# Kernel optimization log

Hardware: AMD Instinct MI355X
Metric: run time of the kernel (lower is better)

## Reference

```python
import jax, jax.numpy as jnp
import numpy as np

N_NODES = 100000
N_EDGES = 1_600_000


def _glorot(key, shape):
    fan_in, fan_out = shape
    s = jnp.sqrt(6.0 / (fan_in + fan_out)).astype(jnp.float32)
    return jax.random.uniform(key, shape, jnp.float32, -1.0, 1.0) * s


def setup_inputs() -> dict:
    key = jax.random.key(0)
    ks = jax.random.split(key, 6)
    x = jax.random.normal(ks[0], (N_NODES, 88), jnp.float32)
    edge_index = jax.random.randint(ks[1], (2, N_EDGES), 0, N_NODES, dtype=jnp.int32)
    return {
        "x": x,
        "W1": _glorot(ks[2], (88, 65)), "b1": jnp.zeros((65,), jnp.float32),
        "W2": _glorot(ks[3], (65, 50)), "b2": jnp.zeros((50,), jnp.float32),
        "W3": _glorot(ks[4], (50, 65)), "b3": jnp.zeros((65,), jnp.float32),
        "W4": _glorot(ks[5], (65, 88)), "b4": jnp.zeros((88,), jnp.float32),
        "edge_index": edge_index,
    }


def _gcn_conv(h, W, b, src, dst, norm, n):
    # PyG GCNConv: transform, then normalized neighbor aggregation (self-loops
    # already folded into src/dst/norm).
    h = h @ W                                  # [N, out]
    msg = h[src] * norm[:, None]               # [E+N, out] gather
    return jax.ops.segment_sum(msg, dst, num_segments=n) + b  # scatter-add


def reference(x, W1, b1, W2, b2, W3, b3, W4, b4, edge_index):
    n = x.shape[0]
    loop = jnp.arange(n, dtype=edge_index.dtype)
    src = jnp.concatenate([edge_index[0], loop])   # add self-loops
    dst = jnp.concatenate([edge_index[1], loop])
    deg = jax.ops.segment_sum(jnp.ones_like(dst, dtype=x.dtype), dst, num_segments=n)
    dinv = jnp.where(deg > 0, jax.lax.rsqrt(deg), 0.0)
    norm = dinv[src] * dinv[dst]                   # D^-1/2 (A+I) D^-1/2 edge weights

    # encoder
    h = jax.nn.relu(_gcn_conv(x, W1, b1, src, dst, norm, n))
    h = _gcn_conv(h, W2, b2, src, dst, norm, n)
    # decoder
    h = jax.nn.relu(_gcn_conv(h, W3, b3, src, dst, norm, n))
    return _gcn_conv(h, W4, b4, src, dst, norm, n)
```

## Files before the change

### kernel.cpp

```cpp
#include <hip/hip_runtime.h>

#define BS 256
#define FB 1024
#define NB 256
#define CHUNK 4096
#define CAP 64
#define LCAP 8192

using half8 = __attribute__((ext_vector_type(8))) _Float16;

template<typename T>
__device__ __forceinline__ void load8f(const T* p, float (&d)[8]) {
    if constexpr (sizeof(T) == 4) {
        float4 a = *(const float4*)p;
        float4 b = *(const float4*)(p + 4);
        d[0] = a.x; d[1] = a.y; d[2] = a.z; d[3] = a.w;
        d[4] = b.x; d[5] = b.y; d[6] = b.z; d[7] = b.w;
    } else {
        half8 v = *(const half8*)p;
        #pragma unroll
        for (int j = 0; j < 8; ++j) d[j] = (float)v[j];
    }
}
template<typename T>
__device__ __forceinline__ void store8f(T* p, const float (&d)[8]) {
    if constexpr (sizeof(T) == 4) {
        *(float4*)p       = make_float4(d[0], d[1], d[2], d[3]);
        *(float4*)(p + 4) = make_float4(d[4], d[5], d[6], d[7]);
    } else {
        half8 h;
        #pragma unroll
        for (int j = 0; j < 8; ++j) h[j] = (_Float16)d[j];
        *(half8*)p = h;
    }
}


__global__ __launch_bounds__(BS) void k_bucket(const int* __restrict__ src, const int* __restrict__ dst,
                                               unsigned* __restrict__ bbuf, int* __restrict__ bcounts,
                                               int E, unsigned long long invB, int bsz) {
    __shared__ int lcnt[NB];
    for (int t = threadIdx.x; t < NB; t += BS) lcnt[t] = 0;
    __syncthreads();
    int base_e = blockIdx.x * CHUNK;
    unsigned* mybuf = bbuf + (size_t)blockIdx.x * NB * CAP;
    #pragma unroll
    for (int j = 0; j < CHUNK / BS; ++j) {
        int e = base_e + j * BS + threadIdx.x;
        if (e < E) {
            int d = dst[e];
            int s = src[e];
            int b = (int)(((unsigned long long)(unsigned)d * invB) >> 40);
            int doff = d - b * bsz;
            int pos = atomicAdd(&lcnt[b], 1);
            if (pos < CAP)
                mybuf[b * CAP + pos] = ((unsigned)doff << 17) | (unsigned)s;
        }
    }
    __syncthreads();
    for (int t = threadIdx.x; t < NB; t += BS)
        bcounts[blockIdx.x * NB + t] = min(lcnt[t], CAP);
}

__global__ __launch_bounds__(FB) void k_cnt(const unsigned* __restrict__ bbuf, const int* __restrict__ bcounts,
                                            int* __restrict__ cnt, int nch, int bsz, int N) {
    __shared__ int lhist[512];
    for (int t = threadIdx.x; t < 512; t += FB) lhist[t] = 0;
    __syncthreads();
    int b = blockIdx.x;
    int lo = b * bsz;
    int total = nch * CAP;
    for (int idx = threadIdx.x; idx < total; idx += FB) {
        int seg = idx >> 6, slot = idx & 63;
        int c = bcounts[seg * NB + b];
        if (slot < c)
            atomicAdd(&lhist[bbuf[((size_t)seg * NB + b) * CAP + slot] >> 17], 1);
    }
    __syncthreads();
    int hi = min(N, lo + bsz);
    for (int t = threadIdx.x; t < hi - lo; t += FB) cnt[lo + t] = lhist[t];
}

__global__ __launch_bounds__(BS) void k_scan1(const int* __restrict__ cnt, int* __restrict__ bsum,
                                              float* __restrict__ dinv, int N) {
    __shared__ int s[BS];
    int i = blockIdx.x * BS + threadIdx.x;
    int v = (i < N) ? cnt[i] : 0;
    if (i < N) dinv[i] = rsqrtf((float)(v + 1));
    s[threadIdx.x] = v;
    __syncthreads();
    for (int off = BS / 2; off > 0; off >>= 1) {
        if (threadIdx.x < off) s[threadIdx.x] += s[threadIdx.x + off];
        __syncthreads();
    }
    if (threadIdx.x == 0) bsum[blockIdx.x] = s[0];
}

__global__ __launch_bounds__(512) void k_scan2(int* bsum, int nb) {
    __shared__ int s[512];
    int t = threadIdx.x;
    int v = (t < nb) ? bsum[t] : 0;
    s[t] = v;
    __syncthreads();
    for (int off = 1; off < 512; off <<= 1) {
        int u = (t >= off) ? s[t - off] : 0;
        __syncthreads();
        s[t] += u;
        __syncthreads();
    }
    if (t < nb) bsum[t] = s[t] - v;
}

__global__ __launch_bounds__(BS) void k_scan3(const int* __restrict__ cnt, const int* __restrict__ boff,
                                              int* __restrict__ row_ptr, int N) {
    __shared__ int s[BS];
    int t = threadIdx.x;
    int i = blockIdx.x * BS + t;
    int v = (i < N) ? cnt[i] : 0;
    s[t] = v;
    __syncthreads();
    for (int off = 1; off < BS; off <<= 1) {
        int u = (t >= off) ? s[t - off] : 0;
        __syncthreads();
        s[t] += u;
        __syncthreads();
    }
    int base = boff[blockIdx.x];
    if (i < N) row_ptr[i] = base + s[t] - v;
    if (i == N - 1) row_ptr[N] = base + s[t];
}

__global__ __launch_bounds__(FB) void k_fill2(const unsigned* __restrict__ bbuf, const int* __restrict__ bcounts,
                                              const int* __restrict__ row_ptr, const float* __restrict__ dinv,
                                              uint2* __restrict__ entries,
                                              int nch, int bsz, int N) {
    __shared__ int cur[512];
    __shared__ float ldinv[512];
    __shared__ unsigned sorted[LCAP];

    int b = blockIdx.x;
    int lo = b * bsz;
    int hi = min(N, lo + bsz);
    int gbase = row_ptr[lo];
    int tot = row_ptr[hi] - gbase;
    for (int t = threadIdx.x; t < hi - lo; t += FB) {
        cur[t] = row_ptr[lo + t] - gbase;
        ldinv[t] = dinv[lo + t];
    }
    __syncthreads();

    int total = nch * CAP;
    for (int idx = threadIdx.x; idx < total; idx += FB) {
        int seg = idx >> 6, slot = idx & 63;
        int c = bcounts[seg * NB + b];
        if (slot < c) {
            unsigned u = bbuf[((size_t)seg * NB + b) * CAP + slot];
            int p = atomicAdd(&cur[u >> 17], 1);
            if (p < LCAP) sorted[p] = u;
        }
    }
    __syncthreads();

    for (int t = threadIdx.x; t < tot; t += FB) {
        unsigned u = sorted[t];
        int s = (int)(u & 0x1FFFFu);
        int doff = (int)(u >> 17);
        float w = dinv[s] * ldinv[doff];
        entries[gbase + t] = make_uint2((unsigned)s, __float_as_uint(w));
    }
}

template<typename TIN, int K, int M, int LDIN, int LDOUT, bool BIAS, bool RELU, typename TOUT>
__global__ __launch_bounds__(BS) void k_gemm(const TIN* __restrict__ H, const float* __restrict__ Wg,
                                             const float* __restrict__ bias, TOUT* __restrict__ out, int N) {
    constexpr int M8 = (M + 7) & ~7;
    constexpr int CG = M8 / 8;
    constexpr int WSTR = K * 8 + 4;
    __shared__ float Wl[CG * WSTR];
    for (int idx = threadIdx.x; idx < CG * WSTR; idx += BS) {
        int cg = idx / WSTR, rem = idx - cg * WSTR;
        int k = rem >> 3, j = rem & 7;
        int m = cg * 8 + j;
        Wl[idx] = (rem < K * 8 && m < M) ? Wg[(size_t)k * M + m] : 0.f;
    }
    __syncthreads();

    int nrq = (N + 3) >> 2;
    int idx = blockIdx.x * BS + threadIdx.x;
    if (idx >= nrq * CG) return;
    int rq = idx / CG;
    int cg = idx - rq * CG;
    int c0 = cg * 8;
    int r0 = rq * 4;
    const float* wb = &Wl[cg * WSTR];

    const TIN* h[4];
    #pragma unroll
    for (int r = 0; r < 4; ++r) {
        int rr = r0 + r; rr = (rr < N) ? rr : (N - 1);
        h[r] = H + (size_t)rr * LDIN;
    }

    float acc[4][8];
    #pragma unroll
    for (int r = 0; r < 4; ++r)
        #pragma unroll
        for (int m = 0; m < 8; ++m) acc[r][m] = 0.f;

    constexpr int K8 = K & ~7;
    #pragma unroll 1
    for (int k = 0; k < K8; k += 8) {
        float p[4][8];
        load8f(h[0] + k, p[0]);
        load8f(h[1] + k, p[1]);
        load8f(h[2] + k, p[2]);
        load8f(h[3] + k, p[3]);
        const float* wl = wb + k * 8;
        #pragma unroll
        for (int j = 0; j < 8; ++j) {
            float4 wa = *(const float4*)(wl + j * 8);
            float4 wc = *(const float4*)(wl + j * 8 + 4);
            const float wv[8] = {wa.x, wa.y, wa.z, wa.w, wc.x, wc.y, wc.z, wc.w};
            #pragma unroll
            for (int r = 0; r < 4; ++r)
                #pragma unroll
                for (int m = 0; m < 8; ++m)
                    acc[r][m] = fmaf(p[r][j], wv[m], acc[r][m]);
        }
    }
    #pragma unroll
    for (int k = K8; k < K; ++k) {
        const float* wl = wb + k * 8;
        float4 wa = *(const float4*)(wl);
        float4 wc = *(const float4*)(wl + 4);
        const float wv[8] = {wa.x, wa.y, wa.z, wa.w, wc.x, wc.y, wc.z, wc.w};
        #pragma unroll
        for (int r = 0; r < 4; ++r) {
            float pv = (float)h[r][k];
            #pragma unroll
            for (int m = 0; m < 8; ++m)
                acc[r][m] = fmaf(pv, wv[m], acc[r][m]);
        }
    }

    #pragma unroll
    for (int r = 0; r < 4; ++r) {
        int rr = r0 + r;
        if (rr >= N) break;
        float v[8];
        #pragma unroll
        for (int m = 0; m < 8; ++m) {
            int c = c0 + m;
            bool in = (c < M);
            float x = in ? acc[r][m] : 0.f;
            if (BIAS && in) x += bias[c];
            if (RELU) x = fmaxf(x, 0.f);
            v[m] = x;
        }
        store8f(out + (size_t)rr * LDOUT + c0, v);
    }
}

template<typename TIN, typename TOUT, int M, int M8, int LDI, int LDO, bool BIAS, bool RELU>
__global__ __launch_bounds__(BS) void k_agg(const TIN* __restrict__ T, TOUT* __restrict__ out,
                                            const int* __restrict__ row_ptr, const uint2* __restrict__ entries,
                                            const float* __restrict__ dinv, const float* __restrict__ bias,
                                            int N) {
    constexpr int CG = M8 / 8;
    int idx = blockIdx.x * BS + threadIdx.x;
    if (idx >= N * CG) return;
    int i  = idx / CG;
    int cg = idx - i * CG;
    int c0 = cg * 8;

    float di = dinv[i];
    float w0 = di * di;
    float t0[8];
    load8f(T + (size_t)i * LDI + c0, t0);
    float a0[8], a1[8];
    #pragma unroll
    for (int m = 0; m < 8; ++m) { a0[m] = w0 * t0[m]; a1[m] = 0.f; }

    int e0 = row_ptr[i], e1 = row_ptr[i + 1];
    for (int e = e0; e < e1; e += 8) {
        unsigned sidx[8];
        float w[8];
        #pragma unroll
        for (int j = 0; j < 8; ++j) {
            int ee = e + j;
            int ec = (ee < e1) ? ee : (e1 - 1);
            uint2 u = entries[ec];
            sidx[j] = u.x;
            w[j] = (ee < e1) ? __uint_as_float(u.y) : 0.f;
        }
        #pragma unroll
        for (int j = 0; j < 8; ++j) {
            float g[8];
            load8f(T + (size_t)sidx[j] * LDI + c0, g);
            if (j & 1) {
                #pragma unroll
                for (int m = 0; m < 8; ++m) a1[m] = fmaf(w[j], g[m], a1[m]);
            } else {
                #pragma unroll
                for (int m = 0; m < 8; ++m) a0[m] = fmaf(w[j], g[m], a0[m]);
            }
        }
    }

    #pragma unroll
    for (int m = 0; m < 8; ++m) {
        float v = a0[m] + a1[m];
        if (BIAS && (c0 + m) < M) v += bias[c0 + m];
        if (RELU) v = fmaxf(v, 0.f);
        a0[m] = v;
    }
    store8f(out + (size_t)i * LDO + c0, a0);
}


extern "C" void kernel_launch(void* const* d_in, const int* in_sizes, int n_in,
                              void* d_out, int out_size, void* d_ws, size_t ws_size,
                              hipStream_t stream) {
    const float* x  = (const float*)d_in[0];
    const float* W1 = (const float*)d_in[1];
    const float* b1 = (const float*)d_in[2];
    const float* W2 = (const float*)d_in[3];
    const float* b2 = (const float*)d_in[4];
    const float* W3 = (const float*)d_in[5];
    const float* b3 = (const float*)d_in[6];
    const float* W4 = (const float*)d_in[7];
    const float* b4 = (const float*)d_in[8];
    const int* edge_index = (const int*)d_in[9];

    const int N = in_sizes[0] / 88;
    const int E = in_sizes[9] / 2;
    const int* src = edge_index;
    const int* dst = edge_index + E;

    const int nch = (E + CHUNK - 1) / CHUNK;
    const int bsz = (N + NB - 1) / NB;
    const unsigned long long invB = ((1ull << 40) + bsz - 1) / bsz;

    auto al = [](size_t b) { return (b + 255) & ~(size_t)255; };
    char* p = (char*)d_ws;
    auto carve = [&](size_t bytes) { void* r = p; p += (bytes + 255) & ~(size_t)255; return r; };
    int*   cnt     = (int*)  carve((size_t)N * 4);
    float* dinv    = (float*)carve((size_t)N * 4);
    int*   row_ptr = (int*)  carve((size_t)(N + 1) * 4);
    int*   bsum    = (int*)  carve(4096);
    uint2* entries = (uint2*)carve((size_t)E * 8);

    char* ub = p;
    int*      bcounts = (int*)ub;
    unsigned* bbuf    = (unsigned*)(ub + al((size_t)nch * NB * 4));
    size_t csr_bytes  = al((size_t)nch * NB * 4) + al((size_t)nch * NB * CAP * 4);

    size_t hbytes = al((size_t)N * 72 * 2);
    _Float16* hA = (_Float16*)ub;
    _Float16* hB = (_Float16*)(ub + hbytes);
    _Float16* hC = (_Float16*)(ub + 2 * hbytes);
    size_t h_bytes_tot = 3 * hbytes;

    p = ub + (csr_bytes > h_bytes_tot ? csr_bytes : h_bytes_tot);
    (void)p; (void)ws_size;

    int gN = (N + BS - 1) / BS;

    k_bucket<<<nch, BS, 0, stream>>>(src, dst, bbuf, bcounts, E, invB, bsz);
    k_cnt   <<<NB, FB, 0, stream>>>(bbuf, bcounts, cnt, nch, bsz, N);
    k_scan1 <<<gN, BS, 0, stream>>>(cnt, bsum, dinv, N);
    k_scan2 <<<1, 512, 0, stream>>>(bsum, gN);
    k_scan3 <<<gN, BS, 0, stream>>>(cnt, bsum, row_ptr, N);
    k_fill2 <<<NB, FB, 0, stream>>>(bbuf, bcounts, row_ptr, dinv, entries, nch, bsz, N);

    auto agg_grid  = [&](int CG) { return (N * CG + BS - 1) / BS; };
    auto gemm_grid = [&](int M)  { int M8 = (M + 7) & ~7; int CG = M8 / 8;
                                   return (((N + 3) / 4) * CG + BS - 1) / BS; };

    k_gemm<float, 88, 65, 88, 72, false, false, _Float16><<<gemm_grid(65), BS, 0, stream>>>(x, W1, nullptr, hA, N);
    k_agg<_Float16, _Float16, 65, 72, 72, 72, true, true><<<agg_grid(9), BS, 0, stream>>>(hA, hB, row_ptr, entries, dinv, b1, N);
    k_gemm<_Float16, 65, 50, 72, 56, false, false, _Float16><<<gemm_grid(50), BS, 0, stream>>>(hB, W2, nullptr, hC, N);
    k_agg<_Float16, _Float16, 50, 56, 56, 56, true, false><<<agg_grid(7), BS, 0, stream>>>(hC, hA, row_ptr, entries, dinv, b2, N);
    k_agg<_Float16, _Float16, 50, 56, 56, 56, false, false><<<agg_grid(7), BS, 0, stream>>>(hA, hB, row_ptr, entries, dinv, nullptr, N);
    k_gemm<_Float16, 50, 65, 56, 72, true, true, _Float16><<<gemm_grid(65), BS, 0, stream>>>(hB, W3, b3, hC, N);
    k_agg<_Float16, _Float16, 65, 72, 72, 72, false, false><<<agg_grid(9), BS, 0, stream>>>(hC, hA, row_ptr, entries, dinv, nullptr, N);
    k_gemm<_Float16, 65, 88, 72, 88, true, false, float><<<gemm_grid(88), BS, 0, stream>>>(hA, W4, b4, (float*)d_out, N);
}
```

Baseline: 456.0 us.

## Fuse neighbor aggregation with following dense transform via shared-memory rows

Adds a k_agg_gemm kernel that aggregates a block of node rows into shared memory and then multiplies them by the next layer's weight matrix before writing, replacing three separate agg+gemm kernel pairs. This removes the global write and re-read of intermediate fp16 feature matrices and cuts the number of launches. It also keeps the aggregated row in fp32 before the GEMM rather than rounding to fp16. Risks include lower occupancy from shared-memory use, idle threads in the GEMM phase, and less parallelism per block. The first GEMM's inner loop is also changed to unroll by 2.

```diff
diff --git a/kernel.cpp b/kernel.cpp
--- a/kernel.cpp
+++ b/kernel.cpp
@@ -208,7 +208,7 @@
         for (int m = 0; m < 8; ++m) acc[r][m] = 0.f;
 
     constexpr int K8 = K & ~7;
-    #pragma unroll 1
+    #pragma unroll 2
     for (int k = 0; k < K8; k += 8) {
         float p[4][8];
         load8f(h[0] + k, p[0]);
@@ -315,6 +315,148 @@
         a0[m] = v;
     }
     store8f(out + (size_t)i * LDO + c0, a0);
+}
+
+template<typename TIN, typename TOUT,
+         int MA, int MA8, int LDI,
+         int MG, int MG8, int LDO,
+         bool ABIAS, bool ARELU, bool GBIAS, bool GRELU>
+__global__ __launch_bounds__(BS) void k_agg_gemm(
+        const TIN* __restrict__ T, TOUT* __restrict__ out,
+        const int* __restrict__ row_ptr, const uint2* __restrict__ entries,
+        const float* __restrict__ dinv, const float* __restrict__ Wg,
+        const float* __restrict__ ab, const float* __restrict__ gb, int N) {
+    constexpr int CGA = MA8 / 8;
+    constexpr int RPB = BS / CGA;
+    constexpr int CGG = MG8 / 8;
+    constexpr int K = MA;
+    constexpr int WSTR = K * 8 + 4;
+
+    __shared__ float Wl[CGG * WSTR];
+    __shared__ float srow[RPB][MA8];
+
+    for (int idx = threadIdx.x; idx < CGG * WSTR; idx += BS) {
+        int cg = idx / WSTR, rem = idx - cg * WSTR;
+        int k = rem >> 3, j = rem & 7;
+        int m = cg * 8 + j;
+        Wl[idx] = (rem < K * 8 && m < MG) ? Wg[(size_t)k * MG + m] : 0.f;
+    }
+
+    int t = threadIdx.x;
+    int r  = t / CGA;
+    int cg = t - r * CGA;
+    int i0 = blockIdx.x * RPB;
+
+    if (r < RPB) {
+        int i = i0 + r;
+        int c0 = cg * 8;
+        if (i < N) {
+            float di = dinv[i];
+            float w0 = di * di;
+            float t0[8];
+            load8f(T + (size_t)i * LDI + c0, t0);
+            float a0[8], a1[8];
+            #pragma unroll
+            for (int m = 0; m < 8; ++m) { a0[m] = w0 * t0[m]; a1[m] = 0.f; }
+
+            int e0 = row_ptr[i], e1 = row_ptr[i + 1];
+            for (int e = e0; e < e1; e += 8) {
+                unsigned sidx[8];
+                float w[8];
+                #pragma unroll
+                for (int j = 0; j < 8; ++j) {
+                    int ee = e + j;
+                    int ec = (ee < e1) ? ee : (e1 - 1);
+                    uint2 u = entries[ec];
+                    sidx[j] = u.x;
+                    w[j] = (ee < e1) ? __uint_as_float(u.y) : 0.f;
+                }
+                #pragma unroll
+                for (int j = 0; j < 8; ++j) {
+                    float g[8];
+                    load8f(T + (size_t)sidx[j] * LDI + c0, g);
+                    if (j & 1) {
+                        #pragma unroll
+                        for (int m = 0; m < 8; ++m) a1[m] = fmaf(w[j], g[m], a1[m]);
+                    } else {
+                        #pragma unroll
+                        for (int m = 0; m < 8; ++m) a0[m] = fmaf(w[j], g[m], a0[m]);
+                    }
+                }
+            }
+            #pragma unroll
+            for (int m = 0; m < 8; ++m) {
+                float v = a0[m] + a1[m];
+                if (ABIAS && (c0 + m) < MA) v += ab[c0 + m];
+                if (ARELU) v = fmaxf(v, 0.f);
+                srow[r][c0 + m] = v;
+            }
+        } else {
+            #pragma unroll
+            for (int m = 0; m < 8; ++m) srow[r][c0 + m] = 0.f;
+        }
+    }
+    __syncthreads();
+
+    for (int ow = t; ow < RPB * CGG; ow += BS) {
+        int orow = ow / CGG;
+        int ocg  = ow - orow * CGG;
+        int gi = i0 + orow;
+        if (gi >= N) continue;
+        const float* hrow = srow[orow];
+        const float* wb = &Wl[ocg * WSTR];
+        float acc[8];
+        #pragma unroll
+        for (int m = 0; m < 8; ++m) acc[m] = 0.f;
+
+        constexpr int K4 = K & ~3;
+        #pragma unroll 2
+        for (int k = 0; k < K4; k += 4) {
+            float4 hv = *(const float4*)(hrow + k);
+            const float h4[4] = {hv.x, hv.y, hv.z, hv.w};
+            #pragma unroll
+            for (int j = 0; j < 4; ++j) {
+                const float* wl = wb + (k + j) * 8;
+                float4 wa = *(const float4*)wl;
+                float4 wc = *(const float4*)(wl + 4);
+                acc[0] = fmaf(h4[j], wa.x, acc[0]);
+                acc[1] = fmaf(h4[j], wa.y, acc[1]);
+                acc[2] = fmaf(h4[j], wa.z, acc[2]);
+                acc[3] = fmaf(h4[j], wa.w, acc[3]);
+                acc[4] = fmaf(h4[j], wc.x, acc[4]);
+                acc[5] = fmaf(h4[j], wc.y, acc[5]);
+                acc[6] = fmaf(h4[j], wc.z, acc[6]);
+                acc[7] = fmaf(h4[j], wc.w, acc[7]);
+            }
+        }
+        #pragma unroll
+        for (int k = K4; k < K; ++k) {
+            float hvv = hrow[k];
+            const float* wl = wb + k * 8;
+            float4 wa = *(const float4*)wl;
+            float4 wc = *(const float4*)(wl + 4);
+            acc[0] = fmaf(hvv, wa.x, acc[0]);
+            acc[1] = fmaf(hvv, wa.y, acc[1]);
+            acc[2] = fmaf(hvv, wa.z, acc[2]);
+            acc[3] = fmaf(hvv, wa.w, acc[3]);
+            acc[4] = fmaf(hvv, wc.x, acc[4]);
+            acc[5] = fmaf(hvv, wc.y, acc[5]);
+            acc[6] = fmaf(hvv, wc.z, acc[6]);
+            acc[7] = fmaf(hvv, wc.w, acc[7]);
+        }
+
+        float v[8];
+        #pragma unroll
+        for (int m = 0; m < 8; ++m) {
+            int c = ocg * 8 + m;
+            bool in = (c < MG);
+            float x = in ? acc[m] : 0.f;
+            if (GBIAS && in) x += gb[c];
+            if (GRELU) x = fmaxf(x, 0.f);
+            v[m] = x;
+        }
+        store8f(out + (size_t)gi * LDO + ocg * 8, v);
+    }
 }
 
 
@@ -357,8 +499,8 @@
 
     size_t hbytes = al((size_t)N * 72 * 2);
     _Float16* hA = (_Float16*)ub;
-    _Float16* hB = (_Float16*)(ub + hbytes);
-    _Float16* hC = (_Float16*)(ub + 2 * hbytes);
+    _Float16* hC = (_Float16*)(ub + hbytes);
+    _Float16* hD = (_Float16*)(ub + 2 * hbytes);
     size_t h_bytes_tot = 3 * hbytes;
 
     p = ub + (csr_bytes > h_bytes_tot ? csr_bytes : h_bytes_tot);
@@ -376,13 +518,17 @@
     auto agg_grid  = [&](int CG) { return (N * CG + BS - 1) / BS; };
     auto gemm_grid = [&](int M)  { int M8 = (M + 7) & ~7; int CG = M8 / 8;
                                    return (((N + 3) / 4) * CG + BS - 1) / BS; };
-
-    k_gemm<float, 88, 65, 88, 72, false, false, _Float16><<<gemm_grid(65), BS, 0, stream>>>(x, W1, nullptr, hA, N);
-    k_agg<_Float16, _Float16, 65, 72, 72, 72, true, true><<<agg_grid(9), BS, 0, stream>>>(hA, hB, row_ptr, entries, dinv, b1, N);
-    k_gemm<_Float16, 65, 50, 72, 56, false, false, _Float16><<<gemm_grid(50), BS, 0, stream>>>(hB, W2, nullptr, hC, N);
-    k_agg<_Float16, _Float16, 50, 56, 56, 56, true, false><<<agg_grid(7), BS, 0, stream>>>(hC, hA, row_ptr, entries, dinv, b2, N);
-    k_agg<_Float16, _Float16, 50, 56, 56, 56, false, false><<<agg_grid(7), BS, 0, stream>>>(hA, hB, row_ptr, entries, dinv, nullptr, N);
-    k_gemm<_Float16, 50, 65, 56, 72, true, true, _Float16><<<gemm_grid(65), BS, 0, stream>>>(hB, W3, b3, hC, N);
-    k_agg<_Float16, _Float16, 65, 72, 72, 72, false, false><<<agg_grid(9), BS, 0, stream>>>(hC, hA, row_ptr, entries, dinv, nullptr, N);
-    k_gemm<_Float16, 65, 88, 72, 88, true, false, float><<<gemm_grid(88), BS, 0, stream>>>(hA, W4, b4, (float*)d_out, N);
-}
+    const int RPB9 = BS / 9;
+    const int RPB7 = BS / 7;
+
+    k_gemm<float, 88, 65, 88, 72, false, false, _Float16>
+        <<<gemm_grid(65), BS, 0, stream>>>(x, W1, nullptr, hA, N);
+    k_agg_gemm<_Float16, _Float16, 65, 72, 72, 50, 56, 56, true, true, false, false>
+        <<<(N + RPB9 - 1) / RPB9, BS, 0, stream>>>(hA, hC, row_ptr, entries, dinv, W2, b1, nullptr, N);
+    k_agg<_Float16, _Float16, 50, 56, 56, 56, true, false>
+        <<<agg_grid(7), BS, 0, stream>>>(hC, hD, row_ptr, entries, dinv, b2, N);
+    k_agg_gemm<_Float16, _Float16, 50, 56, 56, 65, 72, 72, false, false, true, true>
+        <<<(N + RPB7 - 1) / RPB7, BS, 0, stream>>>(hD, hA, row_ptr, entries, dinv, W3, nullptr, b3, N);
+    k_agg_gemm<_Float16, float, 65, 72, 72, 88, 88, 88, false, false, true, false>
+        <<<(N + RPB9 - 1) / RPB9, BS, 0, stream>>>(hA, (float*)d_out, row_ptr, entries, dinv, W4, nullptr, b4, N);
+}
```

After: 449.4 us. About the same (-1.4%).

## Fuse aggregation with following GEMM in persistent software-pipelined kernels

Applied to the files above, without the earlier changes.

Merges the edge bucketing kernel with the first x@W1 GEMM in one launch, splitting the grid between the two jobs so they overlap. Replaces each aggregation+GEMM pair with a persistent kernel that stages aggregated rows in shared memory. The GEMM for the previous tile is interleaved with the gather loop of the current tile, double-buffered across iterations. This removes intermediate global round-trips and several launches, at the cost of large shared-memory use, lower occupancy and a block-wide sync per tile. The second aggregation stays unfused and moves into a separate buffer hD.

```diff
diff --git a/kernel.cpp b/kernel.cpp
--- a/kernel.cpp
+++ b/kernel.cpp
@@ -6,6 +6,7 @@
 #define CHUNK 4096
 #define CAP 64
 #define LCAP 8192
+#define GRID_F 1024
 
 using half8 = __attribute__((ext_vector_type(8))) _Float16;
 
@@ -36,157 +37,54 @@
 }
 
 
-__global__ __launch_bounds__(BS) void k_bucket(const int* __restrict__ src, const int* __restrict__ dst,
-                                               unsigned* __restrict__ bbuf, int* __restrict__ bcounts,
-                                               int E, unsigned long long invB, int bsz) {
-    __shared__ int lcnt[NB];
-    for (int t = threadIdx.x; t < NB; t += BS) lcnt[t] = 0;
-    __syncthreads();
-    int base_e = blockIdx.x * CHUNK;
-    unsigned* mybuf = bbuf + (size_t)blockIdx.x * NB * CAP;
-    #pragma unroll
-    for (int j = 0; j < CHUNK / BS; ++j) {
-        int e = base_e + j * BS + threadIdx.x;
-        if (e < E) {
-            int d = dst[e];
-            int s = src[e];
-            int b = (int)(((unsigned long long)(unsigned)d * invB) >> 40);
-            int doff = d - b * bsz;
-            int pos = atomicAdd(&lcnt[b], 1);
-            if (pos < CAP)
-                mybuf[b * CAP + pos] = ((unsigned)doff << 17) | (unsigned)s;
-        }
-    }
-    __syncthreads();
-    for (int t = threadIdx.x; t < NB; t += BS)
-        bcounts[blockIdx.x * NB + t] = min(lcnt[t], CAP);
-}
-
-__global__ __launch_bounds__(FB) void k_cnt(const unsigned* __restrict__ bbuf, const int* __restrict__ bcounts,
-                                            int* __restrict__ cnt, int nch, int bsz, int N) {
-    __shared__ int lhist[512];
-    for (int t = threadIdx.x; t < 512; t += FB) lhist[t] = 0;
-    __syncthreads();
-    int b = blockIdx.x;
-    int lo = b * bsz;
-    int total = nch * CAP;
-    for (int idx = threadIdx.x; idx < total; idx += FB) {
-        int seg = idx >> 6, slot = idx & 63;
-        int c = bcounts[seg * NB + b];
-        if (slot < c)
-            atomicAdd(&lhist[bbuf[((size_t)seg * NB + b) * CAP + slot] >> 17], 1);
-    }
-    __syncthreads();
-    int hi = min(N, lo + bsz);
-    for (int t = threadIdx.x; t < hi - lo; t += FB) cnt[lo + t] = lhist[t];
-}
-
-__global__ __launch_bounds__(BS) void k_scan1(const int* __restrict__ cnt, int* __restrict__ bsum,
-                                              float* __restrict__ dinv, int N) {
-    __shared__ int s[BS];
-    int i = blockIdx.x * BS + threadIdx.x;
-    int v = (i < N) ? cnt[i] : 0;
-    if (i < N) dinv[i] = rsqrtf((float)(v + 1));
-    s[threadIdx.x] = v;
-    __syncthreads();
-    for (int off = BS / 2; off > 0; off >>= 1) {
-        if (threadIdx.x < off) s[threadIdx.x] += s[threadIdx.x + off];
-        __syncthreads();
-    }
-    if (threadIdx.x == 0) bsum[blockIdx.x] = s[0];
-}
-
-__global__ __launch_bounds__(512) void k_scan2(int* bsum, int nb) {
-    __shared__ int s[512];
-    int t = threadIdx.x;
-    int v = (t < nb) ? bsum[t] : 0;
-    s[t] = v;
-    __syncthreads();
-    for (int off = 1; off < 512; off <<= 1) {
-        int u = (t >= off) ? s[t - off] : 0;
-        __syncthreads();
-        s[t] += u;
-        __syncthreads();
-    }
-    if (t < nb) bsum[t] = s[t] - v;
-}
-
-__global__ __launch_bounds__(BS) void k_scan3(const int* __restrict__ cnt, const int* __restrict__ boff,
-                                              int* __restrict__ row_ptr, int N) {
-    __shared__ int s[BS];
-    int t = threadIdx.x;
-    int i = blockIdx.x * BS + t;
-    int v = (i < N) ? cnt[i] : 0;
-    s[t] = v;
-    __syncthreads();
-    for (int off = 1; off < BS; off <<= 1) {
-        int u = (t >= off) ? s[t - off] : 0;
-        __syncthreads();
-        s[t] += u;
-        __syncthreads();
-    }
-    int base = boff[blockIdx.x];
-    if (i < N) row_ptr[i] = base + s[t] - v;
-    if (i == N - 1) row_ptr[N] = base + s[t];
-}
-
-__global__ __launch_bounds__(FB) void k_fill2(const unsigned* __restrict__ bbuf, const int* __restrict__ bcounts,
-                                              const int* __restrict__ row_ptr, const float* __restrict__ dinv,
-                                              uint2* __restrict__ entries,
-                                              int nch, int bsz, int N) {
-    __shared__ int cur[512];
-    __shared__ float ldinv[512];
-    __shared__ unsigned sorted[LCAP];
-
-    int b = blockIdx.x;
-    int lo = b * bsz;
-    int hi = min(N, lo + bsz);
-    int gbase = row_ptr[lo];
-    int tot = row_ptr[hi] - gbase;
-    for (int t = threadIdx.x; t < hi - lo; t += FB) {
-        cur[t] = row_ptr[lo + t] - gbase;
-        ldinv[t] = dinv[lo + t];
-    }
-    __syncthreads();
-
-    int total = nch * CAP;
-    for (int idx = threadIdx.x; idx < total; idx += FB) {
-        int seg = idx >> 6, slot = idx & 63;
-        int c = bcounts[seg * NB + b];
-        if (slot < c) {
-            unsigned u = bbuf[((size_t)seg * NB + b) * CAP + slot];
-            int p = atomicAdd(&cur[u >> 17], 1);
-            if (p < LCAP) sorted[p] = u;
-        }
-    }
-    __syncthreads();
-
-    for (int t = threadIdx.x; t < tot; t += FB) {
-        unsigned u = sorted[t];
-        int s = (int)(u & 0x1FFFFu);
-        int doff = (int)(u >> 17);
-        float w = dinv[s] * ldinv[doff];
-        entries[gbase + t] = make_uint2((unsigned)s, __float_as_uint(w));
-    }
-}
-
-template<typename TIN, int K, int M, int LDIN, int LDOUT, bool BIAS, bool RELU, typename TOUT>
-__global__ __launch_bounds__(BS) void k_gemm(const TIN* __restrict__ H, const float* __restrict__ Wg,
-                                             const float* __restrict__ bias, TOUT* __restrict__ out, int N) {
-    constexpr int M8 = (M + 7) & ~7;
-    constexpr int CG = M8 / 8;
+__global__ __launch_bounds__(BS) void k_bucket_g1(
+        const int* __restrict__ src, const int* __restrict__ dst,
+        unsigned* __restrict__ bbuf, int* __restrict__ bcounts,
+        int E, unsigned long long invB, int bsz, int nch,
+        const float* __restrict__ x, const float* __restrict__ W1,
+        _Float16* __restrict__ hA, int N) {
+    constexpr int K = 88, M = 65, LDIN = 88, LDOUT = 72;
+    constexpr int CG = 9;
     constexpr int WSTR = K * 8 + 4;
-    __shared__ float Wl[CG * WSTR];
+    __shared__ float sh[CG * WSTR];
+
+    if ((int)blockIdx.x < nch) {
+        int* lcnt = (int*)sh;
+        for (int t = threadIdx.x; t < NB; t += BS) lcnt[t] = 0;
+        __syncthreads();
+        int base_e = blockIdx.x * CHUNK;
+        unsigned* mybuf = bbuf + (size_t)blockIdx.x * NB * CAP;
+        #pragma unroll
+        for (int j = 0; j < CHUNK / BS; ++j) {
+            int e = base_e + j * BS + threadIdx.x;
+            if (e < E) {
+                int d = dst[e];
+                int s = src[e];
+                int b = (int)(((unsigned long long)(unsigned)d * invB) >> 40);
+                int doff = d - b * bsz;
+                int pos = atomicAdd(&lcnt[b], 1);
+                if (pos < CAP)
+                    mybuf[b * CAP + pos] = ((unsigned)doff << 17) | (unsigned)s;
+            }
+        }
+        __syncthreads();
+        for (int t = threadIdx.x; t < NB; t += BS)
+            bcounts[blockIdx.x * NB + t] = min(lcnt[t], CAP);
+        return;
+    }
+
+    float* Wl = sh;
     for (int idx = threadIdx.x; idx < CG * WSTR; idx += BS) {
         int cg = idx / WSTR, rem = idx - cg * WSTR;
         int k = rem >> 3, j = rem & 7;
         int m = cg * 8 + j;
-        Wl[idx] = (rem < K * 8 && m < M) ? Wg[(size_t)k * M + m] : 0.f;
-    }
-    __syncthreads();
-
+        Wl[idx] = (rem < K * 8 && m < M) ? W1[(size_t)k * M + m] : 0.f;
+    }
+    __syncthreads();
+
+    int bid = blockIdx.x - nch;
     int nrq = (N + 3) >> 2;
-    int idx = blockIdx.x * BS + threadIdx.x;
+    int idx = bid * BS + threadIdx.x;
     if (idx >= nrq * CG) return;
     int rq = idx / CG;
     int cg = idx - rq * CG;
@@ -194,22 +92,20 @@
     int r0 = rq * 4;
     const float* wb = &Wl[cg * WSTR];
 
-    const TIN* h[4];
+    const float* h[4];
     #pragma unroll
     for (int r = 0; r < 4; ++r) {
         int rr = r0 + r; rr = (rr < N) ? rr : (N - 1);
-        h[r] = H + (size_t)rr * LDIN;
-    }
-
+        h[r] = x + (size_t)rr * LDIN;
+    }
     float acc[4][8];
     #pragma unroll
     for (int r = 0; r < 4; ++r)
         #pragma unroll
         for (int m = 0; m < 8; ++m) acc[r][m] = 0.f;
 
-    constexpr int K8 = K & ~7;
-    #pragma unroll 1
-    for (int k = 0; k < K8; k += 8) {
+    #pragma unroll 2
+    for (int k = 0; k < K; k += 8) {
         float p[4][8];
         load8f(h[0] + k, p[0]);
         load8f(h[1] + k, p[1]);
@@ -229,21 +125,6 @@
         }
     }
     #pragma unroll
-    for (int k = K8; k < K; ++k) {
-        const float* wl = wb + k * 8;
-        float4 wa = *(const float4*)(wl);
-        float4 wc = *(const float4*)(wl + 4);
-        const float wv[8] = {wa.x, wa.y, wa.z, wa.w, wc.x, wc.y, wc.z, wc.w};
-        #pragma unroll
-        for (int r = 0; r < 4; ++r) {
-            float pv = (float)h[r][k];
-            #pragma unroll
-            for (int m = 0; m < 8; ++m)
-                acc[r][m] = fmaf(pv, wv[m], acc[r][m]);
-        }
-    }
-
-    #pragma unroll
     for (int r = 0; r < 4; ++r) {
         int rr = r0 + r;
         if (rr >= N) break;
@@ -251,13 +132,117 @@
         #pragma unroll
         for (int m = 0; m < 8; ++m) {
             int c = c0 + m;
-            bool in = (c < M);
-            float x = in ? acc[r][m] : 0.f;
-            if (BIAS && in) x += bias[c];
-            if (RELU) x = fmaxf(x, 0.f);
-            v[m] = x;
-        }
-        store8f(out + (size_t)rr * LDOUT + c0, v);
+            v[m] = (c < M) ? acc[r][m] : 0.f;
+        }
+        store8f(hA + (size_t)rr * LDOUT + c0, v);
+    }
+}
+
+__global__ __launch_bounds__(FB) void k_cnt(const unsigned* __restrict__ bbuf, const int* __restrict__ bcounts,
+                                            int* __restrict__ cnt, int nch, int bsz, int N) {
+    __shared__ int lhist[512];
+    for (int t = threadIdx.x; t < 512; t += FB) lhist[t] = 0;
+    __syncthreads();
+    int b = blockIdx.x;
+    int lo = b * bsz;
+    int total = nch * CAP;
+    for (int idx = threadIdx.x; idx < total; idx += FB) {
+        int seg = idx >> 6, slot = idx & 63;
+        int c = bcounts[seg * NB + b];
+        if (slot < c)
+            atomicAdd(&lhist[bbuf[((size_t)seg * NB + b) * CAP + slot] >> 17], 1);
+    }
+    __syncthreads();
+    int hi = min(N, lo + bsz);
+    for (int t = threadIdx.x; t < hi - lo; t += FB) cnt[lo + t] = lhist[t];
+}
+
+__global__ __launch_bounds__(BS) void k_scan1(const int* __restrict__ cnt, int* __restrict__ bsum,
+                                              float* __restrict__ dinv, int N) {
+    __shared__ int s[BS];
+    int i = blockIdx.x * BS + threadIdx.x;
+    int v = (i < N) ? cnt[i] : 0;
+    if (i < N) dinv[i] = rsqrtf((float)(v + 1));
+    s[threadIdx.x] = v;
+    __syncthreads();
+    for (int off = BS / 2; off > 0; off >>= 1) {
+        if (threadIdx.x < off) s[threadIdx.x] += s[threadIdx.x + off];
+        __syncthreads();
+    }
+    if (threadIdx.x == 0) bsum[blockIdx.x] = s[0];
+}
+
+__global__ __launch_bounds__(512) void k_scan2(int* bsum, int nb) {
+    __shared__ int s[512];
+    int t = threadIdx.x;
+    int v = (t < nb) ? bsum[t] : 0;
+    s[t] = v;
+    __syncthreads();
+    for (int off = 1; off < 512; off <<= 1) {
+        int u = (t >= off) ? s[t - off] : 0;
+        __syncthreads();
+        s[t] += u;
+        __syncthreads();
+    }
+    if (t < nb) bsum[t] = s[t] - v;
+}
+
+__global__ __launch_bounds__(BS) void k_scan3(const int* __restrict__ cnt, const int* __restrict__ boff,
+                                              int* __restrict__ row_ptr, int N) {
+    __shared__ int s[BS];
+    int t = threadIdx.x;
+    int i = blockIdx.x * BS + t;
+    int v = (i < N) ? cnt[i] : 0;
+    s[t] = v;
+    __syncthreads();
+    for (int off = 1; off < BS; off <<= 1) {
+        int u = (t >= off) ? s[t - off] : 0;
+        __syncthreads();
+        s[t] += u;
+        __syncthreads();
+    }
+    int base = boff[blockIdx.x];
+    if (i < N) row_ptr[i] = base + s[t] - v;
+    if (i == N - 1) row_ptr[N] = base + s[t];
+}
+
+__global__ __launch_bounds__(FB) void k_fill2(const unsigned* __restrict__ bbuf, const int* __restrict__ bcounts,
+                                              const int* __restrict__ row_ptr, const float* __restrict__ dinv,
+                                              uint2* __restrict__ entries,
+                                              int nch, int bsz, int N) {
+    __shared__ int cur[512];
+    __shared__ float ldinv[512];
+    __shared__ unsigned sorted[LCAP];
+
+    int b = blockIdx.x;
+    int lo = b * bsz;
+    int hi = min(N, lo + bsz);
+    int gbase = row_ptr[lo];
+    int tot = row_ptr[hi] - gbase;
+    for (int t = threadIdx.x; t < hi - lo; t += FB) {
+        cur[t] = row_ptr[lo + t] - gbase;
+        ldinv[t] = dinv[lo + t];
+    }
+    __syncthreads();
+
+    int total = nch * CAP;
+    for (int idx = threadIdx.x; idx < total; idx += FB) {
+        int seg = idx >> 6, slot = idx & 63;
+        int c = bcounts[seg * NB + b];
+        if (slot < c) {
+            unsigned u = bbuf[((size_t)seg * NB + b) * CAP + slot];
+            int p = atomicAdd(&cur[u >> 17], 1);
+            if (p < LCAP) sorted[p] = u;
+        }
+    }
+    __syncthreads();
+
+    for (int t = threadIdx.x; t < tot; t += FB) {
+        unsigned u = sorted[t];
+        int s = (int)(u & 0x1FFFFu);
+        int doff = (int)(u >> 17);
+        float w = dinv[s] * ldinv[doff];
+        entries[gbase + t] = make_uint2((unsigned)s, __float_as_uint(w));
     }
 }
 
@@ -315,6 +300,151 @@
         a0[m] = v;
     }
     store8f(out + (size_t)i * LDO + c0, a0);
+}
+
+template<typename TIN, typename TOUT,
+         int MA, int MA8, int LDI,
+         int MG, int MG8, int LDO,
+         int RPB,
+         bool ABIAS, bool ARELU, bool GBIAS, bool GRELU>
+__global__ __launch_bounds__(BS) void k_agg_gemm(
+        const TIN* __restrict__ T, TOUT* __restrict__ out,
+        const int* __restrict__ row_ptr, const uint2* __restrict__ entries,
+        const float* __restrict__ dinv, const float* __restrict__ Wg,
+        const float* __restrict__ ab, const float* __restrict__ gb, int N) {
+    constexpr int CGA = MA8 / 8;
+    constexpr int CGG = MG8 / 8;
+    constexpr int K = MA;
+    constexpr int WSTR = K * 8 + 4;
+    constexpr int BC = 32;
+
+    __shared__ float Wl[CGG * WSTR];
+    __shared__ float srow[2][RPB][MA8];
+
+    for (int idx = threadIdx.x; idx < CGG * WSTR; idx += BS) {
+        int cg = idx / WSTR, rem = idx - cg * WSTR;
+        int k = rem >> 3, j = rem & 7;
+        int m = cg * 8 + j;
+        Wl[idx] = (rem < K * 8 && m < MG) ? Wg[(size_t)k * MG + m] : 0.f;
+    }
+
+    const int t = threadIdx.x;
+    const int rA = t / CGA, cgA = t - rA * CGA, c0A = cgA * 8;
+    const bool hasA = (rA < RPB);
+    const int rB = t / CGG, cgB = t - rB * CGG, c0B = cgB * 8;
+    const bool hasB = (rB < RPB);
+    const float* wbB = &Wl[cgB * WSTR];
+    const int ntiles = (N + RPB - 1) / RPB;
+
+    for (int s = 0; ; ++s) {
+        int tA = (int)blockIdx.x + s * (int)gridDim.x;
+        int tB = (int)blockIdx.x + (s - 1) * (int)gridDim.x;
+        bool anyA = (tA < ntiles);
+        bool anyB = (s >= 1) && (tB < ntiles);
+        if (!anyA && !anyB) break;
+        int bufA = s & 1, bufB = bufA ^ 1;
+
+        int iA = tA * RPB + rA;
+        bool doA = anyA && hasA && (iA < N);
+        int iB = tB * RPB + rB;
+        bool doB = anyB && hasB && (iB < N);
+
+        float bacc[8];
+        #pragma unroll
+        for (int m = 0; m < 8; ++m) bacc[m] = 0.f;
+        int bk = 0;
+        const float* hrow = &srow[bufB][hasB ? rB : 0][0];
+
+        if (doA) {
+            float di = dinv[iA];
+            float w0 = di * di;
+            float t0[8];
+            load8f(T + (size_t)iA * LDI + c0A, t0);
+            float a0[8], a1[8];
+            #pragma unroll
+            for (int m = 0; m < 8; ++m) { a0[m] = w0 * t0[m]; a1[m] = 0.f; }
+
+            int e0 = row_ptr[iA], e1 = row_ptr[iA + 1];
+            for (int e = e0; e < e1; e += 8) {
+                unsigned sidx[8];
+                float w[8];
+                #pragma unroll
+                for (int j = 0; j < 8; ++j) {
+                    int ee = e + j;
+                    int ec = (ee < e1) ? ee : (e1 - 1);
+                    uint2 u = entries[ec];
+                    sidx[j] = u.x;
+                    w[j] = (ee < e1) ? __uint_as_float(u.y) : 0.f;
+                }
+                float g[8][8];
+                #pragma unroll
+                for (int j = 0; j < 8; ++j)
+                    load8f(T + (size_t)sidx[j] * LDI + c0A, g[j]);
+                if (doB) {
+                    int lim = bk + BC; if (lim > K) lim = K;
+                    for (; bk < lim; ++bk) {
+                        float hv = hrow[bk];
+                        const float* wl = wbB + bk * 8;
+                        float4 wa = *(const float4*)wl;
+                        float4 wc = *(const float4*)(wl + 4);
+                        bacc[0] = fmaf(hv, wa.x, bacc[0]);
+                        bacc[1] = fmaf(hv, wa.y, bacc[1]);
+                        bacc[2] = fmaf(hv, wa.z, bacc[2]);
+                        bacc[3] = fmaf(hv, wa.w, bacc[3]);
+                        bacc[4] = fmaf(hv, wc.x, bacc[4]);
+                        bacc[5] = fmaf(hv, wc.y, bacc[5]);
+                        bacc[6] = fmaf(hv, wc.z, bacc[6]);
+                        bacc[7] = fmaf(hv, wc.w, bacc[7]);
+                    }
+                }
+                #pragma unroll
+                for (int j = 0; j < 8; ++j) {
+                    if (j & 1) {
+                        #pragma unroll
+                        for (int m = 0; m < 8; ++m) a1[m] = fmaf(w[j], g[j][m], a1[m]);
+                    } else {
+                        #pragma unroll
+                        for (int m = 0; m < 8; ++m) a0[m] = fmaf(w[j], g[j][m], a0[m]);
+                    }
+                }
+            }
+            #pragma unroll
+            for (int m = 0; m < 8; ++m) {
+                float v = a0[m] + a1[m];
+                if (ABIAS && (c0A + m) < MA) v += ab[c0A + m];
+                if (ARELU) v = fmaxf(v, 0.f);
+                srow[bufA][rA][c0A + m] = v;
+            }
+        }
+        if (doB) {
+            for (; bk < K; ++bk) {
+                float hv = hrow[bk];
+                const float* wl = wbB + bk * 8;
+                float4 wa = *(const float4*)wl;
+                float4 wc = *(const float4*)(wl + 4);
+                bacc[0] = fmaf(hv, wa.x, bacc[0]);
+                bacc[1] = fmaf(hv, wa.y, bacc[1]);
+                bacc[2] = fmaf(hv, wa.z, bacc[2]);
+                bacc[3] = fmaf(hv, wa.w, bacc[3]);
+                bacc[4] = fmaf(hv, wc.x, bacc[4]);
+                bacc[5] = fmaf(hv, wc.y, bacc[5]);
+                bacc[6] = fmaf(hv, wc.z, bacc[6]);
+                bacc[7] = fmaf(hv, wc.w, bacc[7]);
+            }
+            float v[8];
+            #pragma unroll
+            for (int m = 0; m < 8; ++m) {
+                int c = c0B + m;
+                bool in = (c < MG);
+                float xv = in ? bacc[m] : 0.f;
+                if (GBIAS && in) xv += gb[c];
+                if (GRELU) xv = fmaxf(xv, 0.f);
+                v[m] = xv;
+            }
+            store8f(out + (size_t)iB * LDO + c0B, v);
+        }
+        __syncthreads();
+    }
 }
 
 
@@ -349,6 +479,7 @@
     int*   row_ptr = (int*)  carve((size_t)(N + 1) * 4);
     int*   bsum    = (int*)  carve(4096);
     uint2* entries = (uint2*)carve((size_t)E * 8);
+    _Float16* hA   = (_Float16*)carve((size_t)N * 72 * 2);
 
     char* ub = p;
     int*      bcounts = (int*)ub;
@@ -356,33 +487,32 @@
     size_t csr_bytes  = al((size_t)nch * NB * 4) + al((size_t)nch * NB * CAP * 4);
 
     size_t hbytes = al((size_t)N * 72 * 2);
-    _Float16* hA = (_Float16*)ub;
-    _Float16* hB = (_Float16*)(ub + hbytes);
-    _Float16* hC = (_Float16*)(ub + 2 * hbytes);
-    size_t h_bytes_tot = 3 * hbytes;
+    _Float16* hC = (_Float16*)ub;
+    _Float16* hD = (_Float16*)(ub + hbytes);
+    size_t h_bytes_tot = 2 * hbytes;
 
     p = ub + (csr_bytes > h_bytes_tot ? csr_bytes : h_bytes_tot);
     (void)p; (void)ws_size;
 
     int gN = (N + BS - 1) / BS;
-
-    k_bucket<<<nch, BS, 0, stream>>>(src, dst, bbuf, bcounts, E, invB, bsz);
+    int g1b = (((N + 3) / 4) * 9 + BS - 1) / BS;
+
+    k_bucket_g1<<<nch + g1b, BS, 0, stream>>>(src, dst, bbuf, bcounts, E, invB, bsz, nch,
+                                              x, W1, hA, N);
     k_cnt   <<<NB, FB, 0, stream>>>(bbuf, bcounts, cnt, nch, bsz, N);
     k_scan1 <<<gN, BS, 0, stream>>>(cnt, bsum, dinv, N);
     k_scan2 <<<1, 512, 0, stream>>>(bsum, gN);
     k_scan3 <<<gN, BS, 0, stream>>>(cnt, bsum, row_ptr, N);
     k_fill2 <<<NB, FB, 0, stream>>>(bbuf, bcounts, row_ptr, dinv, entries, nch, bsz, N);
 
-    auto agg_grid  = [&](int CG) { return (N * CG + BS - 1) / BS; };
-    auto gemm_grid = [&](int M)  { int M8 = (M + 7) & ~7; int CG = M8 / 8;
-                                   return (((N + 3) / 4) * CG + BS - 1) / BS; };
-
-    k_gemm<float, 88, 65, 88, 72, false, false, _Float16><<<gemm_grid(65), BS, 0, stream>>>(x, W1, nullptr, hA, N);
-    k_agg<_Float16, _Float16, 65, 72, 72, 72, true, true><<<agg_grid(9), BS, 0, stream>>>(hA, hB, row_ptr, entries, dinv, b1, N);
-    k_gemm<_Float16, 65, 50, 72, 56, false, false, _Float16><<<gemm_grid(50), BS, 0, stream>>>(hB, W2, nullptr, hC, N);
-    k_agg<_Float16, _Float16, 50, 56, 56, 56, true, false><<<agg_grid(7), BS, 0, stream>>>(hC, hA, row_ptr, entries, dinv, b2, N);
-    k_agg<_Float16, _Float16, 50, 56, 56, 56, false, false><<<agg_grid(7), BS, 0, stream>>>(hA, hB, row_ptr, entries, dinv, nullptr, N);
-    k_gemm<_Float16, 50, 65, 56, 72, true, true, _Float16><<<gemm_grid(65), BS, 0, stream>>>(hB, W3, b3, hC, N);
-    k_agg<_Float16, _Float16, 65, 72, 72, 72, false, false><<<agg_grid(9), BS, 0, stream>>>(hC, hA, row_ptr, entries, dinv, nullptr, N);
-    k_gemm<_Float16, 65, 88, 72, 88, true, false, float><<<gemm_grid(88), BS, 0, stream>>>(hA, W4, b4, (float*)d_out, N);
-}
+    auto agg_grid = [&](int CG) { return (N * CG + BS - 1) / BS; };
+
+    k_agg_gemm<_Float16, _Float16, 65, 72, 72, 50, 56, 56, 28, true, true, false, false>
+        <<<GRID_F, BS, 0, stream>>>(hA, hC, row_ptr, entries, dinv, W2, b1, nullptr, N);
+    k_agg<_Float16, _Float16, 50, 56, 56, 56, true, false>
+        <<<agg_grid(7), BS, 0, stream>>>(hC, hD, row_ptr, entries, dinv, b2, N);
+    k_agg_gemm<_Float16, _Float16, 50, 56, 56, 65, 72, 72, 28, false, false, true, true>
+        <<<GRID_F, BS, 0, stream>>>(hD, hA, row_ptr, entries, dinv, W3, nullptr, b3, N);
+    k_agg_gemm<_Float16, float, 65, 72, 72, 88, 88, 88, 23, false, false, true, false>
+        <<<GRID_F, BS, 0, stream>>>(hA, (float*)d_out, row_ptr, entries, dinv, W4, nullptr, b4, N);
+}
```

New measurement: 425.3 us. 1.07x faster.
